# Kernel optimization log

Hardware: AMD Instinct MI355X
Metric: run time of the kernel (lower is better)

Reference implementation:

```python
import jax, jax.numpy as jnp
import numpy as np

B, N, D, H, HD, FF, E, V, HID = 32, 125, 256, 8, 32, 1024, 5, 32000, 128
S = N + 3
MAXPOS = 512
EPS = 1e-12       # BERT LayerNorm eps
THRESH = 0.7


def setup_inputs() -> dict:
    key = jax.random.key(0)
    ks = iter(jax.random.split(key, 32))
    def rn(shape):
        return jax.random.normal(next(ks), shape, jnp.float32)
    def p(shape):
        return rn(shape) * 0.02
    inp = {
        "h_t": rn((B, D)),
        "e_task": rn((B, D)),
        "e_layout": rn((B, D)),
        "token_embeds": rn((B, N, D)),
        # router: Linear(768,128) -> ReLU -> Linear(128,5)
        "router_W1": p((3 * D, HID)), "router_b1": jnp.zeros((HID,), jnp.float32),
        "router_W2": p((HID, E)), "router_b2": jnp.zeros((E,), jnp.float32),
        "hint_W": p((D, E)), "hint_b": jnp.zeros((E,), jnp.float32),
        # per-expert BERT params, stacked over expert dim E
        "pos_emb": p((E, MAXPOS, D)),
        "type_emb": p((E, D)),                    # token_type_id=0 row only
        "ln_emb_g": jnp.ones((E, D), jnp.float32), "ln_emb_b": jnp.zeros((E, D), jnp.float32),
        "Wq": p((E, D, D)), "bq": jnp.zeros((E, D), jnp.float32),
        "Wk": p((E, D, D)), "bk": jnp.zeros((E, D), jnp.float32),
        "Wv": p((E, D, D)), "bv": jnp.zeros((E, D), jnp.float32),
        "Wo": p((E, D, D)), "bo": jnp.zeros((E, D), jnp.float32),
        "ln_attn_g": jnp.ones((E, D), jnp.float32), "ln_attn_b": jnp.zeros((E, D), jnp.float32),
        "Wf1": p((E, D, FF)), "bf1": jnp.zeros((E, FF), jnp.float32),
        "Wf2": p((E, FF, D)), "bf2": jnp.zeros((E, D), jnp.float32),
        "ln_ffn_g": jnp.ones((E, D), jnp.float32), "ln_ffn_b": jnp.zeros((E, D), jnp.float32),
        "head_W": p((D, V)), "head_b": jnp.zeros((V,), jnp.float32),
        "top_k": 2,
    }
    return inp


def _ln(x, g, b):
    m = jnp.mean(x, axis=-1, keepdims=True)
    v = jnp.mean(jnp.square(x - m), axis=-1, keepdims=True)
    return (x - m) * jax.lax.rsqrt(v + EPS) * g + b


def _expert(pos, typ, g0, b0, Wq, bq, Wk, bk, Wv, bv, Wo, bo, g1, b1,
            Wf1, bf1, Wf2, bf2, g2, b2, x):
    # 1-layer BERT encoder (eval mode, no causal mask for inputs_embeds).
    Bx, Sx, _ = x.shape
    h = _ln(x + pos[:Sx][None] + typ[None, None], g0, b0)        # [B,S,D]
    q = (h @ Wq + bq).reshape(Bx, Sx, H, HD)
    k = (h @ Wk + bk).reshape(Bx, Sx, H, HD)
    v = (h @ Wv + bv).reshape(Bx, Sx, H, HD)
    scores = jnp.einsum("bqhd,bkhd->bhqk", q, k) / np.float32(np.sqrt(HD))
    attn = jax.nn.softmax(scores, axis=-1)
    ctx = jnp.einsum("bhqk,bkhd->bqhd", attn, v).reshape(Bx, Sx, D)
    h = _ln(h + ctx @ Wo + bo, g1, b1)
    f = jax.nn.gelu(h @ Wf1 + bf1, approximate=False)
    h = _ln(h + f @ Wf2 + bf2, g2, b2)
    return h


def reference(h_t, e_task, e_layout, token_embeds,
              router_W1, router_b1, router_W2, router_b2, hint_W, hint_b,
              pos_emb, type_emb, ln_emb_g, ln_emb_b,
              Wq, bq, Wk, bk, Wv, bv, Wo, bo, ln_attn_g, ln_attn_b,
              Wf1, bf1, Wf2, bf2, ln_ffn_g, ln_ffn_b,
              head_W, head_b, top_k):
    prefix = jnp.stack([h_t, e_task, e_layout], axis=1)            # [B,3,D]
    x_t = jnp.concatenate([prefix, token_embeds], axis=1)          # [B,S,D]
    flat = jnp.concatenate([h_t, e_task, e_layout], axis=-1)       # [B,3D]
    gate_logits = (jax.nn.relu(flat @ router_W1 + router_b1) @ router_W2
                   + router_b2 + e_layout @ hint_W + hint_b)
    gate_probs = jax.nn.softmax(gate_logits, axis=-1)              # [B,E]
    topk_vals, topk_idx = jax.lax.top_k(gate_probs, top_k)         # [B,k]
    # k collapses to 1 only if EVERY row's max prob exceeds threshold
    use_k1 = jnp.all(jnp.max(gate_probs, axis=-1) > THRESH)
    keep = jnp.where(jnp.arange(top_k) == 0, 1.0,
                     jnp.where(use_k1, 0.0, 1.0)).astype(gate_probs.dtype)
    w = topk_vals * keep[None, :]                                  # [B,k]
    # run all experts densely (E=5 small), then gated combine
    expert_outs = jax.vmap(_expert, in_axes=(0,) * 20 + (None,))(
        pos_emb, type_emb, ln_emb_g, ln_emb_b,
        Wq, bq, Wk, bk, Wv, bv, Wo, bo, ln_attn_g, ln_attn_b,
        Wf1, bf1, Wf2, bf2, ln_ffn_g, ln_ffn_b, x_t)               # [E,B,S,D]
    onehot = jax.nn.one_hot(topk_idx, E, dtype=w.dtype)            # [B,k,E]
    comb = jnp.einsum("bk,bke->be", w, onehot)                     # [B,E]
    z = jnp.einsum("be,ebsd->bsd", comb, expert_outs)              # [B,S,D]
    logits = z @ head_W + head_b                                   # [B,S,V]
    return logits, gate_probs
```

## Files before the change

kernel.cpp:

```cpp
#include <hip/hip_runtime.h>
#include <hip/hip_bf16.h>
#include <math.h>

namespace {

constexpr int B = 32, N = 125, D = 256, H = 8, HD = 32, FF = 1024,
              E = 5, V = 32000, HID = 128, S = 128, MAXPOS = 512;
constexpr int BSD = B * S * D;
constexpr int BSF = B * S * FF;
constexpr float EPS = 1e-12f;
constexpr float THRESH = 0.7f;

constexpr size_t GW_Q = 0, GW_K = 65536, GW_V = 131072, GW_O = 196608,
                 GW_F1 = 262144, GW_F2 = 524288, GW_STRIDE = 786432;

typedef __attribute__((ext_vector_type(4))) float f32x4;
typedef __attribute__((ext_vector_type(8))) short short8v;

__device__ __forceinline__ short f2bf(float f) {
  __hip_bfloat16 h = __float2bfloat16(f);
  short s;
  __builtin_memcpy(&s, &h, 2);
  return s;
}

__device__ __forceinline__ float bf2f(short s) {
  unsigned int u = ((unsigned int)(unsigned short)s) << 16;
  float f;
  __builtin_memcpy(&f, &u, 4);
  return f;
}

__device__ __forceinline__ float gelu_exact(float x) {
  return 0.5f * x * (1.f + erff(x * 0.70710678118654752f));
}

__device__ __forceinline__ float wave_sum64(float v) {
#pragma unroll
  for (int off = 32; off > 0; off >>= 1) v += __shfl_xor(v, off);
  return v;
}

__device__ __forceinline__ void gload16(const void* g, void* l) {
  __builtin_amdgcn_global_load_lds(
      (const __attribute__((address_space(1))) unsigned int*)g,
      (__attribute__((address_space(3))) unsigned int*)l, 16, 0, 0);
}

__global__ __launch_bounds__(HID) void router1_kernel(
    const float* __restrict__ h_t, const float* __restrict__ e_task,
    const float* __restrict__ e_layout, const float* __restrict__ W1,
    const float* __restrict__ b1, const float* __restrict__ W2,
    const float* __restrict__ b2, const float* __restrict__ hintW,
    const float* __restrict__ hintb, float* __restrict__ gp_ws,
    float* __restrict__ gp_out) {
  int b = blockIdx.x;
  int t = threadIdx.x;
  float acc = b1[t];
  const float* rows[3] = {h_t + b * D, e_task + b * D, e_layout + b * D};
  for (int seg = 0; seg < 3; ++seg) {
    const float* r = rows[seg];
    const float* w = W1 + (size_t)seg * D * HID;
    for (int i = 0; i < D; ++i) acc += r[i] * w[i * HID + t];
  }
  __shared__ float hid[HID];
  __shared__ float logits[E];
  hid[t] = fmaxf(acc, 0.f);
  __syncthreads();
  if (t < E) {
    float l = b2[t] + hintb[t];
    for (int hh = 0; hh < HID; ++hh) l += hid[hh] * W2[hh * E + t];
    const float* el = e_layout + b * D;
    for (int dd = 0; dd < D; ++dd) l += el[dd] * hintW[dd * E + t];
    logits[t] = l;
  }
  __syncthreads();
  if (t == 0) {
    float mx = logits[0];
    for (int e2 = 1; e2 < E; ++e2) mx = fmaxf(mx, logits[e2]);
    float p[E];
    float se = 0.f;
    for (int e2 = 0; e2 < E; ++e2) {
      p[e2] = expf(logits[e2] - mx);
      se += p[e2];
    }
    float inv = 1.f / se;
    for (int e2 = 0; e2 < E; ++e2) {
      float pe = p[e2] * inv;
      gp_ws[b * E + e2] = pe;
      gp_out[b * E + e2] = pe;
    }
  }
}

__global__ __launch_bounds__(64) void router2_kernel(
    const float* __restrict__ gp, const int* __restrict__ topk_ptr,
    float* __restrict__ comb) {
  __shared__ int allk1;
  int t = threadIdx.x;
  if (t == 0) allk1 = 1;
  __syncthreads();
  float p[E];
  if (t < B) {
    float mx = 0.f;
    for (int e2 = 0; e2 < E; ++e2) {
      p[e2] = gp[t * E + e2];
      mx = fmaxf(mx, p[e2]);
    }
    if (!(mx > THRESH)) allk1 = 0;
  }
  __syncthreads();
  int k1 = allk1;
  if (t < B) {
    for (int e2 = 0; e2 < E; ++e2) comb[t * E + e2] = 0.f;
    int tk = *topk_ptr;
    if (tk > E) tk = E;
    float q[E];
    for (int e2 = 0; e2 < E; ++e2) q[e2] = p[e2];
    for (int kk = 0; kk < tk; ++kk) {
      int bi = 0;
      float bv = q[0];
      for (int e2 = 1; e2 < E; ++e2)
        if (q[e2] > bv) { bv = q[e2]; bi = e2; }
      float w = (kk == 0) ? bv : (k1 ? 0.f : bv);
      comb[t * E + bi] += w;
      q[bi] = -1.f;
    }
  }
}

__device__ __forceinline__ void prep_body(const float* __restrict__ Wp,
                                          short* __restrict__ Gp, int K,
                                          int Nc) {
  __shared__ float Wl[64][65];
  int t = threadIdx.x;
  int n0 = blockIdx.x * 64, k0 = blockIdx.y * 64;
#pragma unroll
  for (int p = 0; p < 4; ++p) {
    int krow = p * 16 + (t >> 4);
    int nc = (t & 15) * 4;
    float4 v = *reinterpret_cast<const float4*>(
        Wp + (size_t)(k0 + krow) * Nc + n0 + nc);
    Wl[krow][nc] = v.x; Wl[krow][nc + 1] = v.y;
    Wl[krow][nc + 2] = v.z; Wl[krow][nc + 3] = v.w;
  }
  __syncthreads();
#pragma unroll
  for (int p = 0; p < 2; ++p) {
    int gid = p * 256 + t;
    int nl = gid >> 3, kg = gid & 7;
    int xv = (nl >> 1) & 3;
    int bk = kg >> 2, s = kg & 3;
    int sp = s ^ xv;
    short8v o;
#pragma unroll
    for (int j = 0; j < 8; ++j) o[j] = f2bf(Wl[kg * 8 + j][nl]);
    *reinterpret_cast<short8v*>(
        Gp + (size_t)(n0 + nl) * K + ((k0 >> 5) + bk) * 32 + sp * 8) = o;
  }
}

__global__ __launch_bounds__(256) void prep_w(
    const float* __restrict__ W, short* __restrict__ G, int K, int Nc,
    size_t estrW, size_t estrG) {
  int e = blockIdx.z;
  prep_body(W + (size_t)e * estrW, G + (size_t)e * estrG, K, Nc);
}

__global__ __launch_bounds__(256) void prep_experts(
    const float* __restrict__ Wq, const float* __restrict__ Wk,
    const float* __restrict__ Wv, const float* __restrict__ Wo,
    const float* __restrict__ Wf1, const float* __restrict__ Wf2,
    short* __restrict__ Gw) {
  int z = blockIdx.z;
  int e = z / 6, which = z % 6;
  short* Ge = Gw + (size_t)e * GW_STRIDE;
  if (which < 4) {
    if (blockIdx.x >= 4 || blockIdx.y >= 4) return;
    const float* W =
        (which == 0 ? Wq : which == 1 ? Wk : which == 2 ? Wv : Wo) +
        (size_t)e * 65536;
    prep_body(W, Ge + (size_t)which * 65536, 256, 256);
  } else if (which == 4) {
    if (blockIdx.y >= 4) return;
    prep_body(Wf1 + (size_t)e * 262144, Ge + GW_F1, 256, 1024);
  } else {
    if (blockIdx.x >= 4) return;
    prep_body(Wf2 + (size_t)e * 262144, Ge + GW_F2, 1024, 256);
  }
}

__global__ __launch_bounds__(256) void embed_ln_w(
    const float* __restrict__ h_t, const float* __restrict__ e_task,
    const float* __restrict__ e_layout, const float* __restrict__ tok,
    const float* __restrict__ pos_b, const float* __restrict__ typ_b,
    const float* __restrict__ g_b, const float* __restrict__ bb_b,
    short* __restrict__ out_b, const float* __restrict__ comb) {
  int e = blockIdx.y;
  int t = threadIdx.x, lane = t & 63, w = t >> 6;
  int row = blockIdx.x * 4 + w;
  int b = row >> 7, s = row & 127;
  if (comb[b * E + e] == 0.f) return;
  const float* pos_e = pos_b + (size_t)e * MAXPOS * D;
  const float* typ_e = typ_b + (size_t)e * D;
  const float* g = g_b + (size_t)e * D;
  const float* bb = bb_b + (size_t)e * D;
  short* outp = out_b + (size_t)e * BSD;
  int d0 = lane * 4;
  const float* src = (s >= 3) ? tok + ((size_t)(b * N + s - 3)) * D
                   : (s == 0) ? h_t + (size_t)b * D
                   : (s == 1) ? e_task + (size_t)b * D
                              : e_layout + (size_t)b * D;
  float4 x = *reinterpret_cast<const float4*>(src + d0);
  float4 pe = *reinterpret_cast<const float4*>(pos_e + (size_t)s * D + d0);
  float4 te = *reinterpret_cast<const float4*>(typ_e + d0);
  x.x += pe.x + te.x; x.y += pe.y + te.y;
  x.z += pe.z + te.z; x.w += pe.w + te.w;
  float mean = wave_sum64(x.x + x.y + x.z + x.w) * (1.f / D);
  float4 xm = {x.x - mean, x.y - mean, x.z - mean, x.w - mean};
  float vv = wave_sum64(xm.x * xm.x + xm.y * xm.y + xm.z * xm.z + xm.w * xm.w);
  float rs = rsqrtf(vv * (1.f / D) + EPS);
  float4 g4 = *reinterpret_cast<const float4*>(g + d0);
  float4 b4 = *reinterpret_cast<const float4*>(bb + d0);
  short4 o;
  o.x = f2bf(xm.x * rs * g4.x + b4.x);
  o.y = f2bf(xm.y * rs * g4.y + b4.y);
  o.z = f2bf(xm.z * rs * g4.z + b4.z);
  o.w = f2bf(xm.w * rs * g4.w + b4.w);
  *reinterpret_cast<short4*>(outp + (size_t)row * D + d0) = o;
}

__global__ __launch_bounds__(256) void add_ln_w(
    const short* __restrict__ A_b, const short* __restrict__ R_b,
    const float* __restrict__ g_b, const float* __restrict__ bb_b,
    short* __restrict__ out_b, const float* __restrict__ comb) {
  int e = blockIdx.y;
  int t = threadIdx.x, lane = t & 63, w = t >> 6;
  int row = blockIdx.x * 4 + w;
  int b = row >> 7;
  if (comb[b * E + e] == 0.f) return;
  const short* A = A_b + (size_t)e * BSD + (size_t)row * D;
  const short* R = R_b + (size_t)e * BSD + (size_t)row * D;
  const float* g = g_b + (size_t)e * D;
  const float* bb = bb_b + (size_t)e * D;
  short* outp = out_b + (size_t)e * BSD;
  int d0 = lane * 4;
  short4 a4 = *reinterpret_cast<const short4*>(A + d0);
  short4 r4 = *reinterpret_cast<const short4*>(R + d0);
  float4 x = {bf2f(a4.x) + bf2f(r4.x), bf2f(a4.y) + bf2f(r4.y),
              bf2f(a4.z) + bf2f(r4.z), bf2f(a4.w) + bf2f(r4.w)};
  float mean = wave_sum64(x.x + x.y + x.z + x.w) * (1.f / D);
  float4 xm = {x.x - mean, x.y - mean, x.z - mean, x.w - mean};
  float vv = wave_sum64(xm.x * xm.x + xm.y * xm.y + xm.z * xm.z + xm.w * xm.w);
  float rs = rsqrtf(vv * (1.f / D) + EPS);
  float4 g4 = *reinterpret_cast<const float4*>(g + d0);
  float4 b4 = *reinterpret_cast<const float4*>(bb + d0);
  short4 o;
  o.x = f2bf(xm.x * rs * g4.x + b4.x);
  o.y = f2bf(xm.y * rs * g4.y + b4.y);
  o.z = f2bf(xm.z * rs * g4.z + b4.z);
  o.w = f2bf(xm.w * rs * g4.w + b4.w);
  *reinterpret_cast<short4*>(outp + (size_t)row * D + d0) = o;
}

template <int BF16>
__global__ __launch_bounds__(256) void ln2_combine(
    const short* __restrict__ A_b, const short* __restrict__ R_b,
    const float* __restrict__ g_b, const float* __restrict__ bb_b,
    const float* __restrict__ comb, short* __restrict__ zs,
    float* __restrict__ zf) {
  int t = threadIdx.x, lane = t & 63, w = t >> 6;
  int row = blockIdx.x * 4 + w;
  int b = row >> 7;
  int d0 = lane * 4;
  float4 z4 = {0.f, 0.f, 0.f, 0.f};
  for (int e = 0; e < E; ++e) {
    float c = comb[b * E + e];
    if (c == 0.f) continue;
    const short* A = A_b + (size_t)e * BSD + (size_t)row * D;
    const short* R = R_b + (size_t)e * BSD + (size_t)row * D;
    short4 a4 = *reinterpret_cast<const short4*>(A + d0);
    short4 r4 = *reinterpret_cast<const short4*>(R + d0);
    float4 x = {bf2f(a4.x) + bf2f(r4.x), bf2f(a4.y) + bf2f(r4.y),
                bf2f(a4.z) + bf2f(r4.z), bf2f(a4.w) + bf2f(r4.w)};
    float mean = wave_sum64(x.x + x.y + x.z + x.w) * (1.f / D);
    float4 xm = {x.x - mean, x.y - mean, x.z - mean, x.w - mean};
    float vv =
        wave_sum64(xm.x * xm.x + xm.y * xm.y + xm.z * xm.z + xm.w * xm.w);
    float rs = rsqrtf(vv * (1.f / D) + EPS);
    float4 g4 = *reinterpret_cast<const float4*>(g_b + (size_t)e * D + d0);
    float4 b4 = *reinterpret_cast<const float4*>(bb_b + (size_t)e * D + d0);
    z4.x += c * (xm.x * rs * g4.x + b4.x);
    z4.y += c * (xm.y * rs * g4.y + b4.y);
    z4.z += c * (xm.z * rs * g4.z + b4.z);
    z4.w += c * (xm.w * rs * g4.w + b4.w);
  }
  if (BF16) {
    int col = d0;
    int xv = (row >> 1) & 3;
    int colp = (col & ~24) | ((((col >> 3) & 3) ^ xv) << 3);
    short4 o;
    o.x = f2bf(z4.x); o.y = f2bf(z4.y); o.z = f2bf(z4.z); o.w = f2bf(z4.w);
    *reinterpret_cast<short4*>(zs + (size_t)row * 256 + colp) = o;
  } else {
    *reinterpret_cast<float4*>(zf + (size_t)row * D + d0) = z4;
  }
}

__global__ __launch_bounds__(128) void attn2_kernel(
    const short* __restrict__ Qb, const short* __restrict__ Kb,
    const short* __restrict__ Vb, short* __restrict__ Cb,
    const float* __restrict__ comb) {
  int e = blockIdx.y;
  int bh = blockIdx.x;
  int b = bh >> 3, h = bh & 7;
  if (comb[b * E + e] == 0.f) return;
  const short* Q = Qb + (size_t)e * BSD;
  const short* K = Kb + (size_t)e * BSD;
  const short* Vv = Vb + (size_t)e * BSD;
  short* C = Cb + (size_t)e * BSD;
  __shared__ float Ks[S][36];
  __shared__ float Vs[S][36];
  int t = threadIdx.x;
  const short* kbp = K + ((size_t)(b * S + t)) * D + h * HD;
  const short* vbp = Vv + ((size_t)(b * S + t)) * D + h * HD;
#pragma unroll
  for (int j = 0; j < 4; ++j) {
    short8v k8 = *reinterpret_cast<const short8v*>(kbp + j * 8);
    short8v v8 = *reinterpret_cast<const short8v*>(vbp + j * 8);
#pragma unroll
    for (int c = 0; c < 8; ++c) {
      Ks[t][j * 8 + c] = bf2f(k8[c]);
      Vs[t][j * 8 + c] = bf2f(v8[c]);
    }
  }
  float4 qv[8];
  const short* qp = Q + ((size_t)(b * S + t)) * D + h * HD;
#pragma unroll
  for (int j = 0; j < 4; ++j) {
    short8v q8 = *reinterpret_cast<const short8v*>(qp + j * 8);
    qv[j * 2] = (float4){bf2f(q8[0]), bf2f(q8[1]), bf2f(q8[2]), bf2f(q8[3])};
    qv[j * 2 + 1] =
        (float4){bf2f(q8[4]), bf2f(q8[5]), bf2f(q8[6]), bf2f(q8[7])};
  }
  __syncthreads();
  const float scale = 0.17677669529663687f;
  float se = 0.f;
  float4 cx[8];
#pragma unroll
  for (int j = 0; j < 8; ++j) cx[j] = (float4){0.f, 0.f, 0.f, 0.f};
  for (int k = 0; k < S; ++k) {
    float s = 0.f;
#pragma unroll
    for (int j = 0; j < 8; ++j) {
      float4 k4 = *reinterpret_cast<const float4*>(&Ks[k][j * 4]);
      s += qv[j].x * k4.x + qv[j].y * k4.y + qv[j].z * k4.z + qv[j].w * k4.w;
    }
    float p = __expf(s * scale);
    se += p;
#pragma unroll
    for (int j = 0; j < 8; ++j) {
      float4 v4 = *reinterpret_cast<const float4*>(&Vs[k][j * 4]);
      cx[j].x += p * v4.x; cx[j].y += p * v4.y;
      cx[j].z += p * v4.z; cx[j].w += p * v4.w;
    }
  }
  float inv = 1.f / se;
  short* cp = C + ((size_t)(b * S + t)) * D + h * HD;
#pragma unroll
  for (int j = 0; j < 8; ++j) {
    short4 o;
    o.x = f2bf(cx[j].x * inv); o.y = f2bf(cx[j].y * inv);
    o.z = f2bf(cx[j].z * inv); o.w = f2bf(cx[j].w * inv);
    *reinterpret_cast<short4*>(cp + j * 4) = o;
  }
}

template <int ACT, int K, int Nc, int ABF16, int OBF16>
__device__ __forceinline__ void gemm2_body(
    const char* __restrict__ Ag, const short* __restrict__ Gg,
    const float* __restrict__ bias, char* __restrict__ outp, int row0,
    int col0) {
  __shared__ short Al[128 * 40];
  __shared__ short Bl[128 * 32];
  const int t = threadIdx.x;
  const int lane = t & 63;
  const int w = t >> 6;
  const int wr = w >> 1, wc = w & 1;
  const int lrow = lane & 15;
  const int g = lane >> 4;
  const int lkoff = g * 8;
  const int koff = (g ^ ((lrow >> 1) & 3)) << 3;
  const char* Gb = (const char*)Gg;
  char* Bb = (char*)Bl;
  const int srow = t >> 2, sgrp = t & 3;
  const int woff = w * 1024;

  f32x4 acc[4][4];
#pragma unroll
  for (int m = 0; m < 4; ++m)
#pragma unroll
    for (int n = 0; n < 4; ++n) acc[m][n] = (f32x4){0.f, 0.f, 0.f, 0.f};

  for (int k0 = 0; k0 < K; k0 += 32) {
#pragma unroll
    for (int i = 0; i < 2; ++i) {
      int row = i * 64 + srow;
      gload16(Gb + (size_t)(col0 + row) * (K * 2) + (k0 >> 5) * 64 + sgrp * 16,
              Bb + i * 4096 + woff);
    }
    if (ABF16) {
      int row = t >> 1, c0 = (t & 1) * 2;
#pragma unroll
      for (int c = 0; c < 2; ++c) {
        short8v v = *reinterpret_cast<const short8v*>(
            (const short*)Ag + (size_t)(row0 + row) * K + k0 + (c0 + c) * 8);
        *reinterpret_cast<short8v*>(&Al[row * 40 + (c0 + c) * 8]) = v;
      }
    } else {
#pragma unroll
      for (int j = 0; j < 4; ++j) {
        int id = t + 256 * j;
        int row = id >> 3, s4 = id & 7;
        float4 a4 = *reinterpret_cast<const float4*>(
            (const float*)Ag + (size_t)(row0 + row) * K + k0 + s4 * 4);
        short4 p;
        p.x = f2bf(a4.x); p.y = f2bf(a4.y); p.z = f2bf(a4.z); p.w = f2bf(a4.w);
        *reinterpret_cast<short4*>(&Al[row * 40 + s4 * 4]) = p;
      }
    }
    __syncthreads();
    short8v af[4], bfv[4];
#pragma unroll
    for (int m = 0; m < 4; ++m)
      af[m] = *reinterpret_cast<const short8v*>(
          &Al[(wr * 64 + m * 16 + lrow) * 40 + lkoff]);
#pragma unroll
    for (int n = 0; n < 4; ++n)
      bfv[n] = *reinterpret_cast<const short8v*>(
          &Bl[(wc * 64 + n * 16 + lrow) * 32 + koff]);
#pragma unroll
    for (int m = 0; m < 4; ++m)
#pragma unroll
      for (int n = 0; n < 4; ++n)
        acc[m][n] = __builtin_amdgcn_mfma_f32_16x16x32_bf16(
            af[m], bfv[n], acc[m][n], 0, 0, 0);
    __syncthreads();
  }
#pragma unroll
  for (int n = 0; n < 4; ++n) {
    int col = col0 + wc * 64 + n * 16 + lrow;
    float bc = bias[col];
#pragma unroll
    for (int m = 0; m < 4; ++m) {
      int rbase = row0 + wr * 64 + m * 16 + g * 4;
      f32x4 v = acc[m][n];
#pragma unroll
      for (int r = 0; r < 4; ++r) {
        float o = v[r] + bc;
        if (ACT == 1) o = gelu_exact(o);
        if (OBF16)
          ((short*)outp)[(size_t)(rbase + r) * Nc + col] = f2bf(o);
        else
          ((float*)outp)[(size_t)(rbase + r) * Nc + col] = o;
      }
    }
  }
}

template <int ACT, int K, int Nc, int ABF16, int OBF16>
__device__ __forceinline__ void gemm2_body64(
    const char* __restrict__ Ag, const short* __restrict__ Gg,
    const float* __restrict__ bias, char* __restrict__ outp, int row0,
    int col0) {
  __shared__ short Al[64 * 40];
  __shared__ short Bl[128 * 32];
  const int t = threadIdx.x;
  const int lane = t & 63;
  const int w = t >> 6;
  const int lrow = lane & 15;
  const int g = lane >> 4;
  const int lkoff = g * 8;
  const int koff = (g ^ ((lrow >> 1) & 3)) << 3;
  const char* Gb = (const char*)Gg;
  char* Bb = (char*)Bl;
  const int srow = t >> 2, sgrp = t & 3;
  const int woff = w * 1024;

  f32x4 acc[4][2];
#pragma unroll
  for (int m = 0; m < 4; ++m)
#pragma unroll
    for (int n = 0; n < 2; ++n) acc[m][n] = (f32x4){0.f, 0.f, 0.f, 0.f};

  for (int k0 = 0; k0 < K; k0 += 32) {
#pragma unroll
    for (int i = 0; i < 2; ++i) {
      int row = i * 64 + srow;
      gload16(Gb + (size_t)(col0 + row) * (K * 2) + (k0 >> 5) * 64 + sgrp * 16,
              Bb + i * 4096 + woff);
    }
    if (ABF16) {
      int row = t >> 2, seg = t & 3;
      short8v v = *reinterpret_cast<const short8v*>(
          (const short*)Ag + (size_t)(row0 + row) * K + k0 + seg * 8);
      *reinterpret_cast<short8v*>(&Al[row * 40 + seg * 8]) = v;
    } else {
#pragma unroll
      for (int j = 0; j < 2; ++j) {
        int id = t + 256 * j;
        int row = id >> 3, s4 = id & 7;
        float4 a4 = *reinterpret_cast<const float4*>(
            (const float*)Ag + (size_t)(row0 + row) * K + k0 + s4 * 4);
        short4 p;
        p.x = f2bf(a4.x); p.y = f2bf(a4.y); p.z = f2bf(a4.z); p.w = f2bf(a4.w);
        *reinterpret_cast<short4*>(&Al[row * 40 + s4 * 4]) = p;
      }
    }
    __syncthreads();
    short8v af[4], bfv[2];
#pragma unroll
    for (int m = 0; m < 4; ++m)
      af[m] = *reinterpret_cast<const short8v*>(
          &Al[(m * 16 + lrow) * 40 + lkoff]);
#pragma unroll
    for (int n = 0; n < 2; ++n)
      bfv[n] = *reinterpret_cast<const short8v*>(
          &Bl[(w * 32 + n * 16 + lrow) * 32 + koff]);
#pragma unroll
    for (int m = 0; m < 4; ++m)
#pragma unroll
      for (int n = 0; n < 2; ++n)
        acc[m][n] = __builtin_amdgcn_mfma_f32_16x16x32_bf16(
            af[m], bfv[n], acc[m][n], 0, 0, 0);
    __syncthreads();
  }
#pragma unroll
  for (int n = 0; n < 2; ++n) {
    int col = col0 + w * 32 + n * 16 + lrow;
    float bc = bias[col];
#pragma unroll
    for (int m = 0; m < 4; ++m) {
      int rbase = row0 + m * 16 + g * 4;
      f32x4 v = acc[m][n];
#pragma unroll
      for (int r = 0; r < 4; ++r) {
        float o = v[r] + bc;
        if (ACT == 1) o = gelu_exact(o);
        if (OBF16)
          ((short*)outp)[(size_t)(rbase + r) * Nc + col] = f2bf(o);
        else
          ((float*)outp)[(size_t)(rbase + r) * Nc + col] = o;
      }
    }
  }
}

template <int ACT, int K, int Nc, int ABF16, int OBF16>
__global__ __launch_bounds__(256) void gemm2_e(
    const char* __restrict__ Ab, const short* __restrict__ Gbase,
    const float* __restrict__ biasb, char* __restrict__ outb,
    const float* __restrict__ comb, size_t aStrB, size_t oStrB, int bStr) {
  int e = blockIdx.z;
  int row0 = blockIdx.y * 128;
  int col0 = blockIdx.x * 128;
  if (comb[(row0 >> 7) * E + e] == 0.f) return;
  gemm2_body<ACT, K, Nc, ABF16, OBF16>(
      Ab + (size_t)e * aStrB, Gbase + (size_t)e * GW_STRIDE,
      biasb + (size_t)e * bStr, outb + (size_t)e * oStrB, row0, col0);
}

template <int ACT, int K, int Nc, int ABF16, int OBF16>
__global__ __launch_bounds__(256) void gemm2b64_e(
    const char* __restrict__ Ab, const short* __restrict__ Gbase,
    const float* __restrict__ biasb, char* __restrict__ outb,
    const float* __restrict__ comb, size_t aStrB, size_t oStrB, int bStr) {
  int e = blockIdx.z;
  int row0 = blockIdx.y * 64;
  int col0 = blockIdx.x * 128;
  if (comb[(row0 >> 7) * E + e] == 0.f) return;
  gemm2_body64<ACT, K, Nc, ABF16, OBF16>(
      Ab + (size_t)e * aStrB, Gbase + (size_t)e * GW_STRIDE,
      biasb + (size_t)e * bStr, outb + (size_t)e * oStrB, row0, col0);
}

__global__ __launch_bounds__(256) void qkv2_e(
    const short* __restrict__ h0b, const short* __restrict__ Gw,
    const float* __restrict__ bqb, const float* __restrict__ bkb,
    const float* __restrict__ bvb, short* __restrict__ qb,
    short* __restrict__ kb, short* __restrict__ vb,
    const float* __restrict__ comb) {
  int e = blockIdx.z;
  int which = blockIdx.x >> 1;
  int col0 = (blockIdx.x & 1) * 128;
  int row0 = blockIdx.y * 128;
  if (comb[(row0 >> 7) * E + e] == 0.f) return;
  const short* G = Gw + (size_t)e * GW_STRIDE + (size_t)which * 65536;
  const float* bias =
      (which == 0 ? bqb : which == 1 ? bkb : bvb) + (size_t)e * D;
  short* outp = (which == 0 ? qb : which == 1 ? kb : vb) + (size_t)e * BSD;
  gemm2_body<0, D, D, 1, 1>((const char*)(h0b + (size_t)e * BSD), G, bias,
                            (char*)outp, row0, col0);
}

template <int ACT, int K, int Nc>
__device__ __forceinline__ void gemm_body(
    const float* __restrict__ Ag, const float* __restrict__ Wg,
    const float* __restrict__ bias, float* __restrict__ outp, int row0,
    int col0) {
  __shared__ short Al[128 * 40];
  __shared__ short Bl[128 * 40];
  const int t = threadIdx.x;
  const int lane = t & 63;
  const int w = t >> 6;
  const int wr = w >> 1, wc = w & 1;
  const int lrow = lane & 15;
  const int lkoff = (lane >> 4) * 8;
  f32x4 acc[4][4];
#pragma unroll
  for (int m = 0; m < 4; ++m)
#pragma unroll
    for (int n = 0; n < 4; ++n) acc[m][n] = (f32x4){0.f, 0.f, 0.f, 0.f};
  const int colB = t >> 1, kh = (t & 1) * 16;
  for (int k0 = 0; k0 < K; k0 += 32) {
#pragma unroll
    for (int j = 0; j < 4; ++j) {
      int id = t + 256 * j;
      int row = id >> 3, s4 = id & 7;
      float4 a4 = *reinterpret_cast<const float4*>(
          Ag + (size_t)(row0 + row) * K + k0 + s4 * 4);
      short4 p;
      p.x = f2bf(a4.x); p.y = f2bf(a4.y); p.z = f2bf(a4.z); p.w = f2bf(a4.w);
      *reinterpret_cast<short4*>(&Al[row * 40 + s4 * 4]) = p;
    }
    {
      const float* wp = Wg + (size_t)(k0 + kh) * Nc + (col0 + colB);
      short8v v0, v1;
#pragma unroll
      for (int kk = 0; kk < 8; ++kk) v0[kk] = f2bf(wp[(size_t)kk * Nc]);
#pragma unroll
      for (int kk = 0; kk < 8; ++kk) v1[kk] = f2bf(wp[(size_t)(kk + 8) * Nc]);
      *reinterpret_cast<short8v*>(&Bl[colB * 40 + kh]) = v0;
      *reinterpret_cast<short8v*>(&Bl[colB * 40 + kh + 8]) = v1;
    }
    __syncthreads();
    short8v af[4], bfv[4];
#pragma unroll
    for (int m = 0; m < 4; ++m)
      af[m] = *reinterpret_cast<const short8v*>(
          &Al[(wr * 64 + m * 16 + lrow) * 40 + lkoff]);
#pragma unroll
    for (int n = 0; n < 4; ++n)
      bfv[n] = *reinterpret_cast<const short8v*>(
          &Bl[(wc * 64 + n * 16 + lrow) * 40 + lkoff]);
#pragma unroll
    for (int m = 0; m < 4; ++m)
#pragma unroll
      for (int n = 0; n < 4; ++n)
        acc[m][n] = __builtin_amdgcn_mfma_f32_16x16x32_bf16(
            af[m], bfv[n], acc[m][n], 0, 0, 0);
    __syncthreads();
  }
#pragma unroll
  for (int n = 0; n < 4; ++n) {
    int col = col0 + wc * 64 + n * 16 + lrow;
    float bc = bias[col];
#pragma unroll
    for (int m = 0; m < 4; ++m) {
      int rbase = row0 + wr * 64 + m * 16 + (lane >> 4) * 4;
      f32x4 v = acc[m][n];
#pragma unroll
      for (int r = 0; r < 4; ++r) {
        float o = v[r] + bc;
        if (ACT == 1) o = gelu_exact(o);
        outp[(size_t)(rbase + r) * Nc + col] = o;
      }
    }
  }
}

__global__ __launch_bounds__(256) void head_gemm(
    const float* __restrict__ Ag, const float* __restrict__ Wg,
    const float* __restrict__ bias, float* __restrict__ outp) {
  int row0 = blockIdx.x * 128;
  int col0 = blockIdx.y * 128;
  gemm_body<0, D, V>(Ag, Wg, bias, outp, row0, col0);
}

__global__ __launch_bounds__(256) void head_gemm2(
    const short* __restrict__ zs, const short* __restrict__ G,
    const float* __restrict__ bias, float* __restrict__ outp) {
  __shared__ short Al[128 * 32];
  __shared__ short Bl[128 * 32];
  const int row0 = blockIdx.x * 128;
  const int col0 = blockIdx.y * 128;
  const int t = threadIdx.x;
  const int lane = t & 63, w = t >> 6;
  const int wr = w >> 1, wc = w & 1;
  const int lrow = lane & 15;
  const int g = lane >> 4;
  const int koff = (g ^ ((lrow >> 1) & 3)) << 3;
  const int srow = t >> 2, sgrp = t & 3;
  const char* zsb = (const char*)zs;
  const char* Gb = (const char*)G;
  char* Ab = (char*)Al;
  char* Bb = (char*)Bl;
  const int woff = w * 1024;

  f32x4 acc[4][4];
#pragma unroll
  for (int m = 0; m < 4; ++m)
#pragma unroll
    for (int n = 0; n < 4; ++n) acc[m][n] = (f32x4){0.f, 0.f, 0.f, 0.f};

  for (int kb = 0; kb < 8; ++kb) {
#pragma unroll
    for (int i = 0; i < 2; ++i) {
      int row = i * 64 + srow;
      gload16(zsb + (size_t)(row0 + row) * 512 + kb * 64 + sgrp * 16,
              Ab + i * 4096 + woff);
      gload16(Gb + (size_t)(col0 + row) * 512 + kb * 64 + sgrp * 16,
              Bb + i * 4096 + woff);
    }
    __syncthreads();
    short8v af[4], bfv[4];
#pragma unroll
    for (int m = 0; m < 4; ++m)
      af[m] = *reinterpret_cast<const short8v*>(
          &Al[(wr * 64 + m * 16 + lrow) * 32 + koff]);
#pragma unroll
    for (int n = 0; n < 4; ++n)
      bfv[n] = *reinterpret_cast<const short8v*>(
          &Bl[(wc * 64 + n * 16 + lrow) * 32 + koff]);
#pragma unroll
    for (int m = 0; m < 4; ++m)
#pragma unroll
      for (int n = 0; n < 4; ++n)
        acc[m][n] = __builtin_amdgcn_mfma_f32_16x16x32_bf16(
            af[m], bfv[n], acc[m][n], 0, 0, 0);
    __syncthreads();
  }
#pragma unroll
  for (int n = 0; n < 4; ++n) {
    int col = col0 + wc * 64 + n * 16 + lrow;
    float bc = bias[col];
#pragma unroll
    for (int m = 0; m < 4; ++m) {
      int rbase = row0 + wr * 64 + m * 16 + g * 4;
      f32x4 v = acc[m][n];
#pragma unroll
      for (int r = 0; r < 4; ++r)
        outp[(size_t)(rbase + r) * V + col] = v[r] + bc;
    }
  }
}

__global__ __launch_bounds__(256) void combine_f32(
    const short* __restrict__ hb, const float* __restrict__ comb,
    float* __restrict__ zf) {
  size_t i = ((size_t)blockIdx.x * 256 + threadIdx.x) * 4;
  int b = (int)(i >> 15);
  float4 acc = {0.f, 0.f, 0.f, 0.f};
#pragma unroll
  for (int e2 = 0; e2 < E; ++e2) {
    float c = comb[b * E + e2];
    if (c != 0.f) {
      short4 v = *reinterpret_cast<const short4*>(hb + (size_t)e2 * BSD + i);
      acc.x += c * bf2f(v.x); acc.y += c * bf2f(v.y);
      acc.z += c * bf2f(v.z); acc.w += c * bf2f(v.w);
    }
  }
  *reinterpret_cast<float4*>(zf + i) = acc;
}

}

extern "C" void kernel_launch(void* const* d_in, const int* in_sizes, int n_in,
                              void* d_out, int out_size, void* d_ws,
                              size_t ws_size, hipStream_t stream) {
  const float* h_t = (const float*)d_in[0];
  const float* e_task = (const float*)d_in[1];
  const float* e_layout = (const float*)d_in[2];
  const float* tok = (const float*)d_in[3];
  const float* rW1 = (const float*)d_in[4];
  const float* rb1 = (const float*)d_in[5];
  const float* rW2 = (const float*)d_in[6];
  const float* rb2 = (const float*)d_in[7];
  const float* hW = (const float*)d_in[8];
  const float* hb = (const float*)d_in[9];
  const float* pos = (const float*)d_in[10];
  const float* typ = (const float*)d_in[11];
  const float* g0 = (const float*)d_in[12];
  const float* b0 = (const float*)d_in[13];
  const float* Wq = (const float*)d_in[14];
  const float* bq = (const float*)d_in[15];
  const float* Wk = (const float*)d_in[16];
  const float* bk = (const float*)d_in[17];
  const float* Wv = (const float*)d_in[18];
  const float* bv = (const float*)d_in[19];
  const float* Wo = (const float*)d_in[20];
  const float* bo = (const float*)d_in[21];
  const float* g1 = (const float*)d_in[22];
  const float* b1 = (const float*)d_in[23];
  const float* Wf1 = (const float*)d_in[24];
  const float* bf1 = (const float*)d_in[25];
  const float* Wf2 = (const float*)d_in[26];
  const float* bf2 = (const float*)d_in[27];
  const float* g2 = (const float*)d_in[28];
  const float* b2 = (const float*)d_in[29];
  const float* headW = (const float*)d_in[30];
  const float* headb = (const float*)d_in[31];
  const int* topk = (const int*)d_in[32];

  float* out = (float*)d_out;
  float* gp_out = out + (size_t)B * S * V;

  short* h0s = (short*)out;
  short* qs = h0s + (size_t)E * BSD;
  short* ks = qs + (size_t)E * BSD;
  short* vs = ks + (size_t)E * BSD;
  short* ctxs = vs + (size_t)E * BSD;
  short* fbh = ctxs + (size_t)E * BSD;
  short* Gw = fbh + (size_t)E * BSF;

  float* wsf = (float*)d_ws;
  short* Ghead = (short*)d_ws;
  float* comb = wsf + 4096000;
  float* gp = comb + 256;
  short* zs = (short*)(wsf + 4096512);
  size_t need = (size_t)4096512 * 4 + (size_t)4096 * 256 * 2;
  bool fast_head = ws_size >= need;
  if (!fast_head) {
    comb = wsf;
    gp = comb + 256;
  }
  float* zf = gp + 256;

  if (fast_head)
    prep_w<<<dim3(V / 64, 4, 1), 256, 0, stream>>>(headW, Ghead, 256, V, 0, 0);
  prep_experts<<<dim3(16, 16, E * 6), 256, 0, stream>>>(Wq, Wk, Wv, Wo, Wf1,
                                                        Wf2, Gw);

  router1_kernel<<<B, HID, 0, stream>>>(h_t, e_task, e_layout, rW1, rb1, rW2,
                                        rb2, hW, hb, gp, gp_out);
  router2_kernel<<<1, 64, 0, stream>>>(gp, topk, comb);

  dim3 gLN(B * S / 4, E);
  embed_ln_w<<<gLN, 256, 0, stream>>>(h_t, e_task, e_layout, tok, pos, typ,
                                      g0, b0, h0s, comb);
  qkv2_e<<<dim3(6, 32, E), 256, 0, stream>>>(h0s, Gw, bq, bk, bv, qs, ks, vs,
                                             comb);
  attn2_kernel<<<dim3(B * H, E), 128, 0, stream>>>(qs, ks, vs, ctxs, comb);
  gemm2b64_e<0, 256, 256, 1, 1><<<dim3(2, 64, E), 256, 0, stream>>>(
      (const char*)ctxs, Gw + GW_O, bo, (char*)qs, comb, (size_t)BSD * 2,
      (size_t)BSD * 2, 256);
  add_ln_w<<<gLN, 256, 0, stream>>>(h0s, qs, g1, b1, ks, comb);
  gemm2_e<1, 256, 1024, 1, 1><<<dim3(8, 32, E), 256, 0, stream>>>(
      (const char*)ks, Gw + GW_F1, bf1, (char*)fbh, comb, (size_t)BSD * 2,
      (size_t)BSF * 2, FF);
  gemm2b64_e<0, 1024, 256, 1, 1><<<dim3(2, 64, E), 256, 0, stream>>>(
      (const char*)fbh, Gw + GW_F2, bf2, (char*)vs, comb, (size_t)BSF * 2,
      (size_t)BSD * 2, 256);

  if (fast_head) {
    ln2_combine<1><<<B * S / 4, 256, 0, stream>>>(ks, vs, g2, b2, comb, zs,
                                                  nullptr);
    head_gemm2<<<dim3(32, V / 128), 256, 0, stream>>>(zs, Ghead, headb, out);
  } else {
    add_ln_w<<<gLN, 256, 0, stream>>>(ks, vs, g2, b2, h0s, comb);
    combine_f32<<<BSD / 1024, 256, 0, stream>>>(h0s, comb, zf);
    head_gemm<<<dim3(32, V / 128), 256, 0, stream>>>(zf, headW, headb, out);
  }
  (void)in_sizes; (void)n_in; (void)out_size;
}
```

Measured before the change: 375.9 us.

## Fuse attention output projection with residual add and LayerNorm

Replaces the separate Wo GEMM kernel and the add+LayerNorm kernel with one kernel. Each block computes 32 full rows of 256 columns, adds bias and residual, and reduces the row statistics across waves in shared memory. This removes one launch and the bf16 round-trip of the projection output through global memory. In exchange it uses smaller row tiles with no double buffering, so the whole 256-column weight slice is reloaded per block. Variance is computed as E[x²]−mean² instead of the two-pass form.

After: 376.5 us. Within noise of the previous version (+0.2%).

```diff
diff --git a/kernel.cpp b/kernel.cpp
--- a/kernel.cpp
+++ b/kernel.cpp
@@ -376,6 +376,145 @@
   }
 }
 
+__global__ __launch_bounds__(256) void wo_ln(
+    const short* __restrict__ ctxb, const short* __restrict__ Gw,
+    const float* __restrict__ bo_b, const short* __restrict__ h0b,
+    const float* __restrict__ g_b, const float* __restrict__ bb_b,
+    short* __restrict__ out_b, const float* __restrict__ comb) {
+  int e = blockIdx.y;
+  int row0 = blockIdx.x * 32;
+  if (comb[(row0 >> 7) * E + e] == 0.f) return;
+  const short* Ag = ctxb + (size_t)e * BSD;
+  const char* Gb = (const char*)(Gw + (size_t)e * GW_STRIDE + GW_O);
+  const short* R = h0b + (size_t)e * BSD;
+  const float* bo = bo_b + (size_t)e * D;
+  const float* g1 = g_b + (size_t)e * D;
+  const float* b1 = bb_b + (size_t)e * D;
+  short* outp = out_b + (size_t)e * BSD;
+
+  __shared__ short Al[32 * 40];
+  __shared__ short Bl[256 * 32];
+  __shared__ short Rl[32 * 264];
+  __shared__ float redS[4][32];
+  __shared__ float redQ[4][32];
+
+  const int t = threadIdx.x;
+  const int lane = t & 63;
+  const int w = t >> 6;
+  const int lrow = lane & 15;
+  const int g = lane >> 4;
+  const int lkoff = g * 8;
+  const int koff = (g ^ ((lrow >> 1) & 3)) << 3;
+  char* Bb = (char*)Bl;
+  const int woff = w * 1024;
+
+  {
+    int row = t >> 3, seg = t & 7;
+    const short* rp = R + (size_t)(row0 + row) * D + seg * 32;
+#pragma unroll
+    for (int j = 0; j < 4; ++j) {
+      short8v v = *reinterpret_cast<const short8v*>(rp + j * 8);
+      *reinterpret_cast<short8v*>(&Rl[row * 264 + seg * 32 + j * 8]) = v;
+    }
+  }
+
+  f32x4 acc[2][4];
+#pragma unroll
+  for (int m = 0; m < 2; ++m)
+#pragma unroll
+    for (int n = 0; n < 4; ++n) acc[m][n] = (f32x4){0.f, 0.f, 0.f, 0.f};
+
+  for (int k0 = 0; k0 < 256; k0 += 32) {
+#pragma unroll
+    for (int i = 0; i < 4; ++i) {
+      int row = i * 64 + (t >> 2);
+      gload16(Gb + (size_t)row * 512 + (k0 >> 5) * 64 + (t & 3) * 16,
+              Bb + i * 4096 + woff);
+    }
+    if (t < 128) {
+      int row = t >> 2, s4 = t & 3;
+      short8v v = *reinterpret_cast<const short8v*>(
+          Ag + (size_t)(row0 + row) * D + k0 + s4 * 8);
+      *reinterpret_cast<short8v*>(&Al[row * 40 + s4 * 8]) = v;
+    }
+    __syncthreads();
+    short8v af[2], bfv[4];
+#pragma unroll
+    for (int m = 0; m < 2; ++m)
+      af[m] = *reinterpret_cast<const short8v*>(
+          &Al[(m * 16 + lrow) * 40 + lkoff]);
+#pragma unroll
+    for (int n = 0; n < 4; ++n)
+      bfv[n] = *reinterpret_cast<const short8v*>(
+          &Bl[(w * 64 + n * 16 + lrow) * 32 + koff]);
+#pragma unroll
+    for (int m = 0; m < 2; ++m)
+#pragma unroll
+      for (int n = 0; n < 4; ++n)
+        acc[m][n] = __builtin_amdgcn_mfma_f32_16x16x32_bf16(
+            af[m], bfv[n], acc[m][n], 0, 0, 0);
+    __syncthreads();
+  }
+
+  float bo4[4], g4v[4], b4v[4];
+#pragma unroll
+  for (int n = 0; n < 4; ++n) {
+    int col = w * 64 + n * 16 + lrow;
+    bo4[n] = bo[col]; g4v[n] = g1[col]; b4v[n] = b1[col];
+  }
+  float xv0[4][4], xv1[4][4];
+#pragma unroll
+  for (int n = 0; n < 4; ++n) {
+    int col = w * 64 + n * 16 + lrow;
+#pragma unroll
+    for (int r = 0; r < 4; ++r) {
+      xv0[n][r] = acc[0][n][r] + bo4[n] + bf2f(Rl[(g * 4 + r) * 264 + col]);
+      xv1[n][r] =
+          acc[1][n][r] + bo4[n] + bf2f(Rl[(16 + g * 4 + r) * 264 + col]);
+    }
+  }
+#pragma unroll
+  for (int m = 0; m < 2; ++m)
+#pragma unroll
+    for (int r = 0; r < 4; ++r) {
+      float s1 = 0.f, s2 = 0.f;
+#pragma unroll
+      for (int n = 0; n < 4; ++n) {
+        float x = m ? xv1[n][r] : xv0[n][r];
+        s1 += x; s2 += x * x;
+      }
+#pragma unroll
+      for (int off = 1; off < 16; off <<= 1) {
+        s1 += __shfl_xor(s1, off);
+        s2 += __shfl_xor(s2, off);
+      }
+      if (lrow == 0) {
+        int row = m * 16 + g * 4 + r;
+        redS[w][row] = s1;
+        redQ[w][row] = s2;
+      }
+    }
+  __syncthreads();
+#pragma unroll
+  for (int m = 0; m < 2; ++m)
+#pragma unroll
+    for (int r = 0; r < 4; ++r) {
+      int row = m * 16 + g * 4 + r;
+      float Sv = redS[0][row] + redS[1][row] + redS[2][row] + redS[3][row];
+      float Qv = redQ[0][row] + redQ[1][row] + redQ[2][row] + redQ[3][row];
+      float mean = Sv * (1.f / D);
+      float var = Qv * (1.f / D) - mean * mean;
+      float rs = rsqrtf(var + EPS);
+#pragma unroll
+      for (int n = 0; n < 4; ++n) {
+        int col = w * 64 + n * 16 + lrow;
+        float x = m ? xv1[n][r] : xv0[n][r];
+        float o = (x - mean) * rs * g4v[n] + b4v[n];
+        outp[(size_t)(row0 + row) * D + col] = f2bf(o);
+      }
+    }
+}
+
 template <int ACT, int K, int Nc, int ABF16, int OBF16>
 __device__ __forceinline__ void gemm2_body(
     const char* __restrict__ Ag, const short* __restrict__ Gg,
@@ -851,10 +990,8 @@
   qkv2_e<<<dim3(6, 32, E), 256, 0, stream>>>(h0s, Gw, bq, bk, bv, qs, ks, vs,
                                              comb);
   attn2_kernel<<<dim3(B * H, E), 128, 0, stream>>>(qs, ks, vs, ctxs, comb);
-  gemm2b64_e<0, 256, 256, 1, 1><<<dim3(2, 64, E), 256, 0, stream>>>(
-      (const char*)ctxs, Gw + GW_O, bo, (char*)qs, comb, (size_t)BSD * 2,
-      (size_t)BSD * 2, 256);
-  add_ln_w<<<gLN, 256, 0, stream>>>(h0s, qs, g1, b1, ks, comb);
+  wo_ln<<<dim3(128, E), 256, 0, stream>>>(ctxs, Gw, bo, h0s, g1, b1, ks,
+                                          comb);
   gemm2_e<1, 256, 1024, 1, 1><<<dim3(8, 32, E), 256, 0, stream>>>(
       (const char*)ks, Gw + GW_F1, bf1, (char*)fbh, comb, (size_t)BSD * 2,
       (size_t)BSF * 2, FF);
```
